# Kernel optimization log

Hardware: AMD Instinct MI355X
Metric: run time of the kernel (lower is better)

The kernel has to match this reference:

```python
import jax, jax.numpy as jnp
import numpy as np

N, E, F_IN, H, D = 50000, 800000, 256, 4, 128


def _gat_layer(x, W, al, ar, bias, src, dst):
    # x: [N, Fin]; W: [Fin, H*D]; al/ar: [H, D]; bias: [H*D]
    feat = (x @ W).reshape(N, H, D)                      # [N,H,D]
    el = jnp.einsum('nhd,hd->nh', feat, al)              # [N,H]
    er = jnp.einsum('nhd,hd->nh', feat, ar)              # [N,H]
    e = jax.nn.leaky_relu(el[src] + er[dst], negative_slope=0.2)  # [E,H]
    # edge softmax over incoming edges of each dst node (numerically stable)
    emax = jax.ops.segment_max(e, dst, num_segments=N)   # [N,H]
    ee = jnp.exp(e - emax[dst])                          # [E,H]
    denom = jax.ops.segment_sum(ee, dst, num_segments=N) # [N,H]
    a = ee / denom[dst]                                  # [E,H]
    # weighted scatter-aggregate of source features
    out = jax.ops.segment_sum(feat[src] * a[:, :, None], dst, num_segments=N)  # [N,H,D]
    return out + bias.reshape(H, D)


def setup_inputs() -> dict:
    key = jax.random.key(0)
    ks = jax.random.split(key, 16)
    f32 = jnp.float32
    nfeats = jax.random.normal(ks[0], (N, F_IN), dtype=f32)
    src = jax.random.randint(ks[1], (E,), 0, N, dtype=jnp.int32)
    dst = jax.random.randint(ks[2], (E,), 0, N, dtype=jnp.int32)
    def lin(k, fin):
        return jax.random.normal(k, (fin, H * D), dtype=f32) / np.sqrt(fin).astype(np.float32)
    def attn(k):
        return jax.random.normal(k, (H, D), dtype=f32) / np.sqrt(D).astype(np.float32)
    return {
        'nfeats': nfeats,
        'W1': lin(ks[3], F_IN), 'al1': attn(ks[4]), 'ar1': attn(ks[5]), 'b1': jnp.zeros((H * D,), f32),
        'W2': lin(ks[6], D),    'al2': attn(ks[7]), 'ar2': attn(ks[8]), 'b2': jnp.zeros((H * D,), f32),
        'W3': lin(ks[9], D),    'al3': attn(ks[10]), 'ar3': attn(ks[11]), 'b3': jnp.zeros((H * D,), f32),
        'Wc': jax.random.normal(ks[12], (D, 1), dtype=f32) / np.sqrt(D).astype(np.float32),
        'bc': jnp.zeros((1,), f32),
        'src': src, 'dst': dst,
    }


def reference(nfeats, W1, al1, ar1, b1, W2, al2, ar2, b2, W3, al3, ar3, b3, Wc, bc, src, dst):
    h = jnp.mean(jax.nn.relu(_gat_layer(nfeats, W1, al1, ar1, b1, src, dst)), axis=1)  # [N,D]
    h = jnp.mean(jax.nn.relu(_gat_layer(h, W2, al2, ar2, b2, src, dst)), axis=1)
    h = jnp.mean(jax.nn.relu(_gat_layer(h, W3, al3, ar3, b3, src, dst)), axis=1)
    hg = jnp.mean(h, axis=0, keepdims=True)  # readout: mean over nodes -> [1,D]
    return jax.nn.sigmoid(hg @ Wc + bc)      # [1,1]
```

## Files before the change

### kernel.cpp

```cpp
#include <hip/hip_runtime.h>
#include <hip/hip_bf16.h>

#define N_NODES 50000
#define E_EDGES 800000
#define HD 512
#define H_HEADS 4
#define D_DIM 128
#define N_PAD 53248

typedef __attribute__((ext_vector_type(8))) short bf16x8;
typedef __attribute__((ext_vector_type(4))) float f32x4;
typedef __attribute__((ext_vector_type(2))) float f32x2;

__device__ __forceinline__ unsigned short f2b(float f) {
  unsigned u = __float_as_uint(f);
  u += 0x7FFFu + ((u >> 16) & 1u);
  return (unsigned short)(u >> 16);
}
__device__ __forceinline__ float b2f(unsigned short s) {
  return __uint_as_float(((unsigned)s) << 16);
}
__device__ __forceinline__ float lrelu(float v) { return v > 0.f ? v : 0.2f * v; }
__device__ __forceinline__ float sel4(float a, float b, float c, float d, int h) {
  return h == 0 ? a : (h == 1 ? b : (h == 2 ? c : d));
}

#define GLOAD_LDS16(g, l)                                             \
  __builtin_amdgcn_global_load_lds(                                   \
      (const __attribute__((address_space(1))) void*)(g),             \
      (__attribute__((address_space(3))) void*)(l), 16, 0, 0)

__global__ void cast_f2b(const float* __restrict__ in, unsigned short* __restrict__ out, int n4) {
  int i = blockIdx.x * blockDim.x + threadIdx.x;
  if (i >= n4) return;
  float4 v = *(const float4*)(in + (size_t)i * 4);
  ushort4 o;
  o.x = f2b(v.x); o.y = f2b(v.y); o.z = f2b(v.z); o.w = f2b(v.w);
  *(ushort4*)(out + (size_t)i * 4) = o;
}

__global__ void transpose_cast(const float* __restrict__ W, unsigned short* __restrict__ WT, int K) {
  int idx = blockIdx.x * blockDim.x + threadIdx.x;
  if (idx >= K * HD) return;
  int k = idx >> 9, c = idx & (HD - 1);
  WT[(size_t)c * K + k] = f2b(W[idx]);
}

__global__ __launch_bounds__(256) void gemm_mfma(const unsigned short* __restrict__ X,
                                                 const unsigned short* __restrict__ WT,
                                                 unsigned short* __restrict__ feat, int K) {
  __shared__ unsigned short Atile[128 * 64];
  __shared__ unsigned short Btile[128 * 64];
  const int tid = threadIdx.x;
  const int w = tid >> 6, l = tid & 63;
  const int wr = w >> 1, wc = w & 1;
  const int row0 = blockIdx.x * 128;
  const int col0 = blockIdx.y * 128;
  const int fr = l & 15;
  const int fk = (l >> 4) * 8;
  f32x4 acc[4][4] = {};

  for (int k0 = 0; k0 < K; k0 += 64) {
#pragma unroll
    for (int j = 0; j < 4; ++j) {
      int idx = j * 256 + tid;
      int row = idx >> 3;
      int ksw = ((idx & 7) << 3) ^ ((row & 7) << 3);
      int arow = row0 + row;
      if (arow >= N_NODES) arow = N_NODES - 1;
      GLOAD_LDS16(X + (size_t)arow * K + k0 + ksw,
                  (char*)Atile + j * 4096 + w * 1024);
      GLOAD_LDS16(WT + (size_t)(col0 + row) * K + k0 + ksw,
                  (char*)Btile + j * 4096 + w * 1024);
    }
    __syncthreads();
#pragma unroll
    for (int kk = 0; kk < 64; kk += 32) {
      const int kel2 = (kk + fk) * 2;
      bf16x8 af[4], bf[4];
#pragma unroll
      for (int m = 0; m < 4; ++m) {
        int arow = wr * 64 + m * 16 + fr;
        af[m] = *(const bf16x8*)((const char*)Atile + arow * 128 + (kel2 ^ ((arow & 7) << 4)));
        int bcol = wc * 64 + m * 16 + fr;
        bf[m] = *(const bf16x8*)((const char*)Btile + bcol * 128 + (kel2 ^ ((bcol & 7) << 4)));
      }
#pragma unroll
      for (int m = 0; m < 4; ++m)
#pragma unroll
        for (int n = 0; n < 4; ++n)
          acc[m][n] = __builtin_amdgcn_mfma_f32_16x16x32_bf16(af[m], bf[n], acc[m][n], 0, 0, 0);
    }
    __syncthreads();
  }

  const int orow = row0 + wr * 64 + (l >> 4) * 4;
#pragma unroll
  for (int m = 0; m < 4; ++m) {
#pragma unroll
    for (int i = 0; i < 4; ++i) {
      int r = orow + m * 16 + i;
      if (r < N_NODES) {
#pragma unroll
        for (int n = 0; n < 4; ++n)
          feat[(size_t)r * HD + col0 + wc * 64 + n * 16 + fr] = f2b(acc[m][n][i]);
      }
    }
  }
}

__global__ __launch_bounds__(64) void eler_cast(const unsigned short* __restrict__ feat,
                                                const float* __restrict__ al,
                                                const float* __restrict__ ar,
                                                float* __restrict__ el, float* __restrict__ er,
                                                unsigned char* __restrict__ featq) {
  const int n = blockIdx.x, t = threadIdx.x;
  const int h = t >> 4, d0 = (t & 15) * 8;
  uint4 raw = *(const uint4*)(feat + (size_t)n * HD + t * 8);
  unsigned rw[4] = {raw.x, raw.y, raw.z, raw.w};
  float fv[8];
#pragma unroll
  for (int i = 0; i < 4; ++i) {
    fv[2 * i] = b2f((unsigned short)(rw[i] & 0xFFFFu));
    fv[2 * i + 1] = b2f((unsigned short)(rw[i] >> 16));
  }
  const float* alh = al + h * D_DIM + d0;
  const float* arh = ar + h * D_DIM + d0;
  float4 a0 = *(const float4*)alh, a1 = *(const float4*)(alh + 4);
  float4 r0 = *(const float4*)arh, r1 = *(const float4*)(arh + 4);
  float av[8] = {a0.x, a0.y, a0.z, a0.w, a1.x, a1.y, a1.z, a1.w};
  float rv[8] = {r0.x, r0.y, r0.z, r0.w, r1.x, r1.y, r1.z, r1.w};
  float sl = 0.f, sr = 0.f;
#pragma unroll
  for (int i = 0; i < 8; ++i) {
    sl = fmaf(fv[i], av[i], sl);
    sr = fmaf(fv[i], rv[i], sr);
  }
#pragma unroll
  for (int o = 1; o < 16; o <<= 1) {
    sl += __shfl_xor(sl, o);
    sr += __shfl_xor(sr, o);
  }
  if ((t & 15) == 0) {
    el[n * 4 + h] = sl;
    er[n * 4 + h] = sr;
  }
  int q0 = __builtin_amdgcn_cvt_pk_fp8_f32(fv[0], fv[1], 0, false);
  q0 = __builtin_amdgcn_cvt_pk_fp8_f32(fv[2], fv[3], q0, true);
  int q1 = __builtin_amdgcn_cvt_pk_fp8_f32(fv[4], fv[5], 0, false);
  q1 = __builtin_amdgcn_cvt_pk_fp8_f32(fv[6], fv[7], q1, true);
  uint2 qq;
  qq.x = (unsigned)q0;
  qq.y = (unsigned)q1;
  *(uint2*)(featq + (size_t)n * HD + t * 8) = qq;
}

__global__ void histo_kernel(const int* __restrict__ dst, unsigned* __restrict__ deg) {
  int e = blockIdx.x * blockDim.x + threadIdx.x;
  if (e >= E_EDGES) return;
  atomicAdd(&deg[dst[e]], 1u);
}

__global__ void scan_kernel(const unsigned* __restrict__ deg, unsigned* __restrict__ off,
                            unsigned* __restrict__ cursor) {
  __shared__ unsigned warp_sums[16];
  __shared__ unsigned carry_s;
  const int tid = threadIdx.x;
  const int wid = tid >> 6;
  if (tid == 0) carry_s = 0;
  __syncthreads();
  for (int base = 0; base < N_PAD; base += 4096) {
    int i = base + tid * 4;
    uint4 v = *(const uint4*)(deg + i);
    unsigned sm = v.x + v.y + v.z + v.w;
    unsigned x = sm;
#pragma unroll
    for (int o = 1; o < 64; o <<= 1) {
      unsigned y = __shfl_up(x, o);
      if ((tid & 63) >= o) x += y;
    }
    if ((tid & 63) == 63) warp_sums[wid] = x;
    __syncthreads();
    if (tid < 16) {
      unsigned s = warp_sums[tid];
#pragma unroll
      for (int o = 1; o < 16; o <<= 1) {
        unsigned y = __shfl_up(s, o);
        if (tid >= o) s += y;
      }
      warp_sums[tid] = s;
    }
    __syncthreads();
    unsigned carry = carry_s;
    unsigned wprev = (wid > 0) ? warp_sums[wid - 1] : 0u;
    unsigned ex = carry + wprev + (x - sm);
    uint4 o4;
    o4.x = ex;
    o4.y = ex + v.x;
    o4.z = o4.y + v.y;
    o4.w = o4.z + v.z;
    *(uint4*)(off + i) = o4;
    *(uint4*)(cursor + i) = o4;
    __syncthreads();
    if (tid == 0) carry_s = carry + warp_sums[15];
    __syncthreads();
  }
}

__global__ void scatter_kernel(const int* __restrict__ src, const int* __restrict__ dst,
                               unsigned* __restrict__ cursor, int* __restrict__ csr_src) {
  int e = blockIdx.x * blockDim.x + threadIdx.x;
  if (e >= E_EDGES) return;
  int d = dst[e];
  unsigned pos = atomicAdd(&cursor[d], 1u);
  csr_src[pos] = src[e];
}

__global__ __launch_bounds__(64) void agg_fused(const unsigned* __restrict__ off,
                                                const int* __restrict__ csr_src,
                                                const float* __restrict__ el,
                                                const float* __restrict__ er,
                                                const unsigned char* __restrict__ featq,
                                                const float* __restrict__ bias,
                                                unsigned short* __restrict__ hbuf) {
  __shared__ float4 ws4[64];
  const int n = blockIdx.x, t = threadIdx.x;
  const int h = t >> 4, d0 = (t & 15) * 8;
  const unsigned beg = off[n];
  const int deg = (int)(off[n + 1] - beg);
  const float NEG = -3.0e38f;
  float4 rr = *(const float4*)(er + (size_t)n * 4);
  float acc[8] = {};

  if (deg <= 64) {
    float4 v = {NEG, NEG, NEG, NEG};
    if (t < deg) {
      int s = csr_src[beg + t];
      float4 ll = *(const float4*)(el + (size_t)s * 4);
      v.x = lrelu(ll.x + rr.x);
      v.y = lrelu(ll.y + rr.y);
      v.z = lrelu(ll.z + rr.z);
      v.w = lrelu(ll.w + rr.w);
    }
    float m0 = v.x, m1 = v.y, m2 = v.z, m3 = v.w;
#pragma unroll
    for (int o = 32; o >= 1; o >>= 1) {
      m0 = fmaxf(m0, __shfl_xor(m0, o));
      m1 = fmaxf(m1, __shfl_xor(m1, o));
      m2 = fmaxf(m2, __shfl_xor(m2, o));
      m3 = fmaxf(m3, __shfl_xor(m3, o));
    }
    float4 ev = {0.f, 0.f, 0.f, 0.f};
    if (t < deg) {
      ev.x = __expf(v.x - m0);
      ev.y = __expf(v.y - m1);
      ev.z = __expf(v.z - m2);
      ev.w = __expf(v.w - m3);
    }
    float s0 = ev.x, s1 = ev.y, s2 = ev.z, s3 = ev.w;
#pragma unroll
    for (int o = 32; o >= 1; o >>= 1) {
      s0 += __shfl_xor(s0, o);
      s1 += __shfl_xor(s1, o);
      s2 += __shfl_xor(s2, o);
      s3 += __shfl_xor(s3, o);
    }
    if (t < deg) ws4[t] = ev;
    float invh = 1.0f / sel4(s0, s1, s2, s3, h);
    __syncthreads();
    int sj = (deg > 0) ? csr_src[beg] : 0;
    for (int j = 0; j < deg; ++j) {
      int sn = csr_src[beg + ((j + 1 < deg) ? j + 1 : j)];
      float4 wv = ws4[j];
      float w = sel4(wv.x, wv.y, wv.z, wv.w, h) * invh;
      uint2 q = *(const uint2*)(featq + (size_t)sj * HD + t * 8);
      f32x2 p0 = __builtin_amdgcn_cvt_pk_f32_fp8((int)q.x, false);
      f32x2 p1 = __builtin_amdgcn_cvt_pk_f32_fp8((int)q.x, true);
      f32x2 p2 = __builtin_amdgcn_cvt_pk_f32_fp8((int)q.y, false);
      f32x2 p3 = __builtin_amdgcn_cvt_pk_f32_fp8((int)q.y, true);
      acc[0] = fmaf(p0[0], w, acc[0]);
      acc[1] = fmaf(p0[1], w, acc[1]);
      acc[2] = fmaf(p1[0], w, acc[2]);
      acc[3] = fmaf(p1[1], w, acc[3]);
      acc[4] = fmaf(p2[0], w, acc[4]);
      acc[5] = fmaf(p2[1], w, acc[5]);
      acc[6] = fmaf(p3[0], w, acc[6]);
      acc[7] = fmaf(p3[1], w, acc[7]);
      sj = sn;
    }
  } else {
    float m[4] = {NEG, NEG, NEG, NEG};
    for (int j = t; j < deg; j += 64) {
      int s = csr_src[beg + j];
      float4 ll = *(const float4*)(el + (size_t)s * 4);
      m[0] = fmaxf(m[0], lrelu(ll.x + rr.x));
      m[1] = fmaxf(m[1], lrelu(ll.y + rr.y));
      m[2] = fmaxf(m[2], lrelu(ll.z + rr.z));
      m[3] = fmaxf(m[3], lrelu(ll.w + rr.w));
    }
#pragma unroll
    for (int o = 32; o >= 1; o >>= 1) {
      m[0] = fmaxf(m[0], __shfl_xor(m[0], o));
      m[1] = fmaxf(m[1], __shfl_xor(m[1], o));
      m[2] = fmaxf(m[2], __shfl_xor(m[2], o));
      m[3] = fmaxf(m[3], __shfl_xor(m[3], o));
    }
    float sm[4] = {0.f, 0.f, 0.f, 0.f};
    for (int j = t; j < deg; j += 64) {
      int s = csr_src[beg + j];
      float4 ll = *(const float4*)(el + (size_t)s * 4);
      sm[0] += __expf(lrelu(ll.x + rr.x) - m[0]);
      sm[1] += __expf(lrelu(ll.y + rr.y) - m[1]);
      sm[2] += __expf(lrelu(ll.z + rr.z) - m[2]);
      sm[3] += __expf(lrelu(ll.w + rr.w) - m[3]);
    }
#pragma unroll
    for (int o = 32; o >= 1; o >>= 1) {
      sm[0] += __shfl_xor(sm[0], o);
      sm[1] += __shfl_xor(sm[1], o);
      sm[2] += __shfl_xor(sm[2], o);
      sm[3] += __shfl_xor(sm[3], o);
    }
    float mh = sel4(m[0], m[1], m[2], m[3], h);
    float ih = 1.0f / sel4(sm[0], sm[1], sm[2], sm[3], h);
    float rrh = sel4(rr.x, rr.y, rr.z, rr.w, h);
    for (int j = 0; j < deg; ++j) {
      int sj = csr_src[beg + j];
      float llh = el[(size_t)sj * 4 + h];
      float w = __expf(lrelu(llh + rrh) - mh) * ih;
      uint2 q = *(const uint2*)(featq + (size_t)sj * HD + t * 8);
      f32x2 p0 = __builtin_amdgcn_cvt_pk_f32_fp8((int)q.x, false);
      f32x2 p1 = __builtin_amdgcn_cvt_pk_f32_fp8((int)q.x, true);
      f32x2 p2 = __builtin_amdgcn_cvt_pk_f32_fp8((int)q.y, false);
      f32x2 p3 = __builtin_amdgcn_cvt_pk_f32_fp8((int)q.y, true);
      acc[0] = fmaf(p0[0], w, acc[0]);
      acc[1] = fmaf(p0[1], w, acc[1]);
      acc[2] = fmaf(p1[0], w, acc[2]);
      acc[3] = fmaf(p1[1], w, acc[3]);
      acc[4] = fmaf(p2[0], w, acc[4]);
      acc[5] = fmaf(p2[1], w, acc[5]);
      acc[6] = fmaf(p3[0], w, acc[6]);
      acc[7] = fmaf(p3[1], w, acc[7]);
    }
  }

  const float* bp = bias + h * D_DIM + d0;
  float4 b0 = *(const float4*)bp, b1 = *(const float4*)(bp + 4);
  float bv[8] = {b0.x, b0.y, b0.z, b0.w, b1.x, b1.y, b1.z, b1.w};
  float r[8];
#pragma unroll
  for (int i = 0; i < 8; ++i) r[i] = fmaxf(acc[i] + bv[i], 0.f);
#pragma unroll
  for (int i = 0; i < 8; ++i) {
    r[i] += __shfl_xor(r[i], 16);
    r[i] += __shfl_xor(r[i], 32);
  }
  if (h == 0) {
    uint4 o;
    o.x = (unsigned)f2b(r[0] * 0.25f) | ((unsigned)f2b(r[1] * 0.25f) << 16);
    o.y = (unsigned)f2b(r[2] * 0.25f) | ((unsigned)f2b(r[3] * 0.25f) << 16);
    o.z = (unsigned)f2b(r[4] * 0.25f) | ((unsigned)f2b(r[5] * 0.25f) << 16);
    o.w = (unsigned)f2b(r[6] * 0.25f) | ((unsigned)f2b(r[7] * 0.25f) << 16);
    *(uint4*)(hbuf + (size_t)n * D_DIM + d0) = o;
  }
}

__global__ void colsum(const unsigned short* __restrict__ hbuf, float* __restrict__ hg) {
  int d = threadIdx.x;
  float s = 0.0f;
  for (int n = blockIdx.x; n < N_NODES; n += gridDim.x)
    s += b2f(hbuf[(size_t)n * D_DIM + d]);
  atomicAdd(&hg[d], s);
}

__global__ void final_k(const float* __restrict__ hg, const float* __restrict__ Wc,
                        const float* __restrict__ bc, float* __restrict__ out) {
  int l = threadIdx.x;
  float v = hg[l] * Wc[l] + hg[l + 64] * Wc[l + 64];
#pragma unroll
  for (int off = 32; off >= 1; off >>= 1) v += __shfl_xor(v, off);
  if (l == 0) {
    float x = v * (1.0f / N_NODES) + bc[0];
    out[0] = 1.0f / (1.0f + expf(-x));
  }
}

extern "C" void kernel_launch(void* const* d_in, const int* in_sizes, int n_in,
                              void* d_out, int out_size, void* d_ws, size_t ws_size,
                              hipStream_t stream) {
  const float* nfeats = (const float*)d_in[0];
  const float* W1 = (const float*)d_in[1];
  const float* al1 = (const float*)d_in[2];
  const float* ar1 = (const float*)d_in[3];
  const float* b1 = (const float*)d_in[4];
  const float* W2 = (const float*)d_in[5];
  const float* al2 = (const float*)d_in[6];
  const float* ar2 = (const float*)d_in[7];
  const float* b2 = (const float*)d_in[8];
  const float* W3 = (const float*)d_in[9];
  const float* al3 = (const float*)d_in[10];
  const float* ar3 = (const float*)d_in[11];
  const float* b3 = (const float*)d_in[12];
  const float* Wc = (const float*)d_in[13];
  const float* bc = (const float*)d_in[14];
  const int* src = (const int*)d_in[15];
  const int* dst = (const int*)d_in[16];
  float* out = (float*)d_out;

  char* p = (char*)d_ws;
  auto carve = [&](size_t bytes) {
    char* r = p;
    p += (bytes + 255) & ~(size_t)255;
    return r;
  };
  float* el = (float*)carve((size_t)N_NODES * 4 * 4);
  float* er = (float*)carve((size_t)N_NODES * 4 * 4);
  float* hg = (float*)carve(512);
  unsigned* deg = (unsigned*)carve((size_t)N_PAD * 4);
  unsigned* offv = (unsigned*)carve((size_t)(N_PAD + 4) * 4);
  unsigned* cursor = (unsigned*)carve((size_t)N_PAD * 4);
  int* csr_src = (int*)carve((size_t)E_EDGES * 4);
  unsigned short* featb = (unsigned short*)carve((size_t)N_NODES * HD * 2);
  unsigned char* featq = (unsigned char*)carve((size_t)N_NODES * HD);
  unsigned short* hbufb = (unsigned short*)carve((size_t)N_NODES * D_DIM * 2);
  unsigned short* xb = (unsigned short*)carve((size_t)(N_NODES + 128) * 256 * 2);
  unsigned short* WT1 = (unsigned short*)carve((size_t)HD * 256 * 2);
  unsigned short* WT2 = (unsigned short*)carve((size_t)HD * 128 * 2);
  unsigned short* WT3 = (unsigned short*)carve((size_t)HD * 128 * 2);

  hipMemsetAsync(deg, 0, (size_t)N_PAD * sizeof(unsigned), stream);
  histo_kernel<<<(E_EDGES + 255) / 256, 256, 0, stream>>>(dst, deg);
  scan_kernel<<<1, 1024, 0, stream>>>(deg, offv, cursor);
  scatter_kernel<<<(E_EDGES + 255) / 256, 256, 0, stream>>>(src, dst, cursor, csr_src);

  cast_f2b<<<(N_NODES * 256 / 4 + 255) / 256, 256, 0, stream>>>(nfeats, xb, N_NODES * 256 / 4);
  transpose_cast<<<(256 * HD + 255) / 256, 256, 0, stream>>>(W1, WT1, 256);
  transpose_cast<<<(128 * HD + 255) / 256, 256, 0, stream>>>(W2, WT2, 128);
  transpose_cast<<<(128 * HD + 255) / 256, 256, 0, stream>>>(W3, WT3, 128);

  auto run_layer = [&](const unsigned short* X, int K, const unsigned short* WT,
                       const float* alv, const float* arv, const float* bv) {
    dim3 g((N_NODES + 127) / 128, HD / 128);
    gemm_mfma<<<g, 256, 0, stream>>>(X, WT, featb, K);
    eler_cast<<<N_NODES, 64, 0, stream>>>(featb, alv, arv, el, er, featq);
    agg_fused<<<N_NODES, 64, 0, stream>>>(offv, csr_src, el, er, featq, bv, hbufb);
  };

  run_layer(xb, 256, WT1, al1, ar1, b1);
  run_layer(hbufb, 128, WT2, al2, ar2, b2);
  run_layer(hbufb, 128, WT3, al3, ar3, b3);

  hipMemsetAsync(hg, 0, 512, stream);
  colsum<<<1024, 128, 0, stream>>>(hbufb, hg);
  final_k<<<1, 64, 0, stream>>>(hg, Wc, bc, out);
}
```

Baseline: 491.9 us.

## Fold attention vectors into weights, quantize GEMM output to fp8 directly, unroll aggregation

Precomputes W·al and W·ar per layer so el/er come from a small GEMV over the input features, and deletes the eler_cast kernel along with the bf16 feature buffer. The GEMM epilogue now writes fp8 features directly, cutting a full write and re-read of the bf16 feature matrix. The low-degree aggregation loop is unrolled by 4 with independent gathers and packed f32x2 FMAs to raise memory-level parallelism. The GEMM now stores single bytes, which may coalesce poorly, and el/er are computed from bf16 inputs instead of bf16-rounded features, which slightly changes the numerics.

```diff
diff --git a/kernel.cpp b/kernel.cpp
--- a/kernel.cpp
+++ b/kernel.cpp
@@ -23,6 +23,9 @@
 __device__ __forceinline__ float lrelu(float v) { return v > 0.f ? v : 0.2f * v; }
 __device__ __forceinline__ float sel4(float a, float b, float c, float d, int h) {
   return h == 0 ? a : (h == 1 ? b : (h == 2 ? c : d));
+}
+__device__ __forceinline__ float sel4v(float4 v, int h) {
+  return sel4(v.x, v.y, v.z, v.w, h);
 }
 
 #define GLOAD_LDS16(g, l)                                             \
@@ -46,9 +49,71 @@
   WT[(size_t)c * K + k] = f2b(W[idx]);
 }
 
+__global__ void compute_wal(const float* __restrict__ W, const float* __restrict__ al,
+                            const float* __restrict__ ar, float* __restrict__ wal, int K) {
+  int idx = blockIdx.x * blockDim.x + threadIdx.x;
+  if (idx >= K * 8) return;
+  int k = idx >> 3, j = idx & 7, h = j >> 1;
+  const float* a = ((j & 1) ? ar : al) + h * D_DIM;
+  const float* w = W + (size_t)k * HD + h * D_DIM;
+  float s = 0.f;
+  for (int d = 0; d < D_DIM; d += 4) {
+    float4 wv = *(const float4*)(w + d);
+    float4 av = *(const float4*)(a + d);
+    s = fmaf(wv.x, av.x, s);
+    s = fmaf(wv.y, av.y, s);
+    s = fmaf(wv.z, av.z, s);
+    s = fmaf(wv.w, av.w, s);
+  }
+  wal[idx] = s;
+}
+
+__global__ __launch_bounds__(256) void gemv_eler(const unsigned short* __restrict__ X,
+                                                 const float* __restrict__ wal,
+                                                 float* __restrict__ el, float* __restrict__ er,
+                                                 int K) {
+  const int t = threadIdx.x;
+  const int u = (t & 63) >> 3, v = t & 7;
+  const int wave = t >> 6;
+  const int n0 = blockIdx.x * 32 + wave * 8 + u;
+  int n = (n0 < N_NODES) ? n0 : N_NODES - 1;
+  const int kc = K >> 3;
+  const unsigned short* xp = X + (size_t)n * K + v * kc;
+  float acc[8] = {};
+  for (int k = 0; k < kc; k += 8) {
+    bf16x8 xv = *(const bf16x8*)(xp + k);
+    int kg = v * kc + k;
+#pragma unroll
+    for (int i = 0; i < 8; ++i) {
+      float xf = b2f((unsigned short)xv[i]);
+      float4 w0 = *(const float4*)(wal + (size_t)(kg + i) * 8);
+      float4 w1 = *(const float4*)(wal + (size_t)(kg + i) * 8 + 4);
+      acc[0] = fmaf(xf, w0.x, acc[0]);
+      acc[1] = fmaf(xf, w0.y, acc[1]);
+      acc[2] = fmaf(xf, w0.z, acc[2]);
+      acc[3] = fmaf(xf, w0.w, acc[3]);
+      acc[4] = fmaf(xf, w1.x, acc[4]);
+      acc[5] = fmaf(xf, w1.y, acc[5]);
+      acc[6] = fmaf(xf, w1.z, acc[6]);
+      acc[7] = fmaf(xf, w1.w, acc[7]);
+    }
+  }
+#pragma unroll
+  for (int o = 1; o < 8; o <<= 1) {
+#pragma unroll
+    for (int j = 0; j < 8; ++j) acc[j] += __shfl_xor(acc[j], o);
+  }
+  if (v == 0 && n0 < N_NODES) {
+    float4 elv = {acc[0], acc[2], acc[4], acc[6]};
+    float4 erv = {acc[1], acc[3], acc[5], acc[7]};
+    *(float4*)(el + (size_t)n0 * 4) = elv;
+    *(float4*)(er + (size_t)n0 * 4) = erv;
+  }
+}
+
 __global__ __launch_bounds__(256) void gemm_mfma(const unsigned short* __restrict__ X,
                                                  const unsigned short* __restrict__ WT,
-                                                 unsigned short* __restrict__ feat, int K) {
+                                                 unsigned char* __restrict__ featq, int K) {
   __shared__ unsigned short Atile[128 * 64];
   __shared__ unsigned short Btile[128 * 64];
   const int tid = threadIdx.x;
@@ -94,65 +159,22 @@
     __syncthreads();
   }
 
-  const int orow = row0 + wr * 64 + (l >> 4) * 4;
+  const int g = l >> 4;
+  const int col_base = col0 + wc * 64;
 #pragma unroll
   for (int m = 0; m < 4; ++m) {
 #pragma unroll
     for (int i = 0; i < 4; ++i) {
-      int r = orow + m * 16 + i;
+      int r = row0 + wr * 64 + m * 16 + g * 4 + i;
       if (r < N_NODES) {
 #pragma unroll
-        for (int n = 0; n < 4; ++n)
-          feat[(size_t)r * HD + col0 + wc * 64 + n * 16 + fr] = f2b(acc[m][n][i]);
+        for (int n = 0; n < 4; ++n) {
+          int b = __builtin_amdgcn_cvt_pk_fp8_f32(acc[m][n][i], acc[m][n][i], 0, false);
+          featq[(size_t)r * HD + col_base + n * 16 + fr] = (unsigned char)(b & 0xFF);
+        }
       }
     }
   }
-}
-
-__global__ __launch_bounds__(64) void eler_cast(const unsigned short* __restrict__ feat,
-                                                const float* __restrict__ al,
-                                                const float* __restrict__ ar,
-                                                float* __restrict__ el, float* __restrict__ er,
-                                                unsigned char* __restrict__ featq) {
-  const int n = blockIdx.x, t = threadIdx.x;
-  const int h = t >> 4, d0 = (t & 15) * 8;
-  uint4 raw = *(const uint4*)(feat + (size_t)n * HD + t * 8);
-  unsigned rw[4] = {raw.x, raw.y, raw.z, raw.w};
-  float fv[8];
-#pragma unroll
-  for (int i = 0; i < 4; ++i) {
-    fv[2 * i] = b2f((unsigned short)(rw[i] & 0xFFFFu));
-    fv[2 * i + 1] = b2f((unsigned short)(rw[i] >> 16));
-  }
-  const float* alh = al + h * D_DIM + d0;
-  const float* arh = ar + h * D_DIM + d0;
-  float4 a0 = *(const float4*)alh, a1 = *(const float4*)(alh + 4);
-  float4 r0 = *(const float4*)arh, r1 = *(const float4*)(arh + 4);
-  float av[8] = {a0.x, a0.y, a0.z, a0.w, a1.x, a1.y, a1.z, a1.w};
-  float rv[8] = {r0.x, r0.y, r0.z, r0.w, r1.x, r1.y, r1.z, r1.w};
-  float sl = 0.f, sr = 0.f;
-#pragma unroll
-  for (int i = 0; i < 8; ++i) {
-    sl = fmaf(fv[i], av[i], sl);
-    sr = fmaf(fv[i], rv[i], sr);
-  }
-#pragma unroll
-  for (int o = 1; o < 16; o <<= 1) {
-    sl += __shfl_xor(sl, o);
-    sr += __shfl_xor(sr, o);
-  }
-  if ((t & 15) == 0) {
-    el[n * 4 + h] = sl;
-    er[n * 4 + h] = sr;
-  }
-  int q0 = __builtin_amdgcn_cvt_pk_fp8_f32(fv[0], fv[1], 0, false);
-  q0 = __builtin_amdgcn_cvt_pk_fp8_f32(fv[2], fv[3], q0, true);
-  int q1 = __builtin_amdgcn_cvt_pk_fp8_f32(fv[4], fv[5], 0, false);
-  q1 = __builtin_amdgcn_cvt_pk_fp8_f32(fv[6], fv[7], q1, true);
-  uint2 qq;
-  qq.x = (unsigned)q0;
-  qq.y = (unsigned)q1;
-  *(uint2*)(featq + (size_t)n * HD + t * 8) = qq;
 }
 
 __global__ void histo_kernel(const int* __restrict__ dst, unsigned* __restrict__ deg) {
@@ -230,7 +252,7 @@
   const int deg = (int)(off[n + 1] - beg);
   const float NEG = -3.0e38f;
   float4 rr = *(const float4*)(er + (size_t)n * 4);
-  float acc[8] = {};
+  f32x2 acc2[4] = {};
 
   if (deg <= 64) {
     float4 v = {NEG, NEG, NEG, NEG};
@@ -265,28 +287,48 @@
       s2 += __shfl_xor(s2, o);
       s3 += __shfl_xor(s3, o);
     }
-    if (t < deg) ws4[t] = ev;
+    ws4[t] = ev;
     float invh = 1.0f / sel4(s0, s1, s2, s3, h);
     __syncthreads();
-    int sj = (deg > 0) ? csr_src[beg] : 0;
-    for (int j = 0; j < deg; ++j) {
-      int sn = csr_src[beg + ((j + 1 < deg) ? j + 1 : j)];
-      float4 wv = ws4[j];
-      float w = sel4(wv.x, wv.y, wv.z, wv.w, h) * invh;
-      uint2 q = *(const uint2*)(featq + (size_t)sj * HD + t * 8);
-      f32x2 p0 = __builtin_amdgcn_cvt_pk_f32_fp8((int)q.x, false);
-      f32x2 p1 = __builtin_amdgcn_cvt_pk_f32_fp8((int)q.x, true);
-      f32x2 p2 = __builtin_amdgcn_cvt_pk_f32_fp8((int)q.y, false);
-      f32x2 p3 = __builtin_amdgcn_cvt_pk_f32_fp8((int)q.y, true);
-      acc[0] = fmaf(p0[0], w, acc[0]);
-      acc[1] = fmaf(p0[1], w, acc[1]);
-      acc[2] = fmaf(p1[0], w, acc[2]);
-      acc[3] = fmaf(p1[1], w, acc[3]);
-      acc[4] = fmaf(p2[0], w, acc[4]);
-      acc[5] = fmaf(p2[1], w, acc[5]);
-      acc[6] = fmaf(p3[0], w, acc[6]);
-      acc[7] = fmaf(p3[1], w, acc[7]);
-      sj = sn;
+    const unsigned char* fq = featq + t * 8;
+    for (int j0 = 0; j0 < deg; j0 += 4) {
+      int i1 = (j0 + 1 < deg) ? j0 + 1 : j0;
+      int i2 = (j0 + 2 < deg) ? j0 + 2 : j0;
+      int i3 = (j0 + 3 < deg) ? j0 + 3 : j0;
+      int sa = csr_src[beg + j0], sb = csr_src[beg + i1];
+      int sc = csr_src[beg + i2], sd = csr_src[beg + i3];
+      uint2 qa = *(const uint2*)(fq + (size_t)sa * HD);
+      uint2 qb = *(const uint2*)(fq + (size_t)sb * HD);
+      uint2 qc = *(const uint2*)(fq + (size_t)sc * HD);
+      uint2 qd = *(const uint2*)(fq + (size_t)sd * HD);
+      float wa = sel4v(ws4[j0], h) * invh;
+      float wb = sel4v(ws4[i1], h) * invh;
+      float wc2 = sel4v(ws4[i2], h) * invh;
+      float wd = sel4v(ws4[i3], h) * invh;
+      if (j0 + 1 >= deg) wb = 0.f;
+      if (j0 + 2 >= deg) wc2 = 0.f;
+      if (j0 + 3 >= deg) wd = 0.f;
+      f32x2 w2;
+      w2 = (f32x2){wa, wa};
+      acc2[0] += __builtin_amdgcn_cvt_pk_f32_fp8((int)qa.x, false) * w2;
+      acc2[1] += __builtin_amdgcn_cvt_pk_f32_fp8((int)qa.x, true) * w2;
+      acc2[2] += __builtin_amdgcn_cvt_pk_f32_fp8((int)qa.y, false) * w2;
+      acc2[3] += __builtin_amdgcn_cvt_pk_f32_fp8((int)qa.y, true) * w2;
+      w2 = (f32x2){wb, wb};
+      acc2[0] += __builtin_amdgcn_cvt_pk_f32_fp8((int)qb.x, false) * w2;
+      acc2[1] += __builtin_amdgcn_cvt_pk_f32_fp8((int)qb.x, true) * w2;
+      acc2[2] += __builtin_amdgcn_cvt_pk_f32_fp8((int)qb.y, false) * w2;
+      acc2[3] += __builtin_amdgcn_cvt_pk_f32_fp8((int)qb.y, true) * w2;
+      w2 = (f32x2){wc2, wc2};
+      acc2[0] += __builtin_amdgcn_cvt_pk_f32_fp8((int)qc.x, false) * w2;
+      acc2[1] += __builtin_amdgcn_cvt_pk_f32_fp8((int)qc.x, true) * w2;
+      acc2[2] += __builtin_amdgcn_cvt_pk_f32_fp8((int)qc.y, false) * w2;
+      acc2[3] += __builtin_amdgcn_cvt_pk_f32_fp8((int)qc.y, true) * w2;
+      w2 = (f32x2){wd, wd};
+      acc2[0] += __builtin_amdgcn_cvt_pk_f32_fp8((int)qd.x, false) * w2;
+      acc2[1] += __builtin_amdgcn_cvt_pk_f32_fp8((int)qd.x, true) * w2;
+      acc2[2] += __builtin_amdgcn_cvt_pk_f32_fp8((int)qd.y, false) * w2;
+      acc2[3] += __builtin_amdgcn_cvt_pk_f32_fp8((int)qd.y, true) * w2;
     }
   } else {
     float m[4] = {NEG, NEG, NEG, NEG};
@@ -329,18 +371,11 @@
       float llh = el[(size_t)sj * 4 + h];
       float w = __expf(lrelu(llh + rrh) - mh) * ih;
       uint2 q = *(const uint2*)(featq + (size_t)sj * HD + t * 8);
-      f32x2 p0 = __builtin_amdgcn_cvt_pk_f32_fp8((int)q.x, false);
-      f32x2 p1 = __builtin_amdgcn_cvt_pk_f32_fp8((int)q.x, true);
-      f32x2 p2 = __builtin_amdgcn_cvt_pk_f32_fp8((int)q.y, false);
-      f32x2 p3 = __builtin_amdgcn_cvt_pk_f32_fp8((int)q.y, true);
-      acc[0] = fmaf(p0[0], w, acc[0]);
-      acc[1] = fmaf(p0[1], w, acc[1]);
-      acc[2] = fmaf(p1[0], w, acc[2]);
-      acc[3] = fmaf(p1[1], w, acc[3]);
-      acc[4] = fmaf(p2[0], w, acc[4]);
-      acc[5] = fmaf(p2[1], w, acc[5]);
-      acc[6] = fmaf(p3[0], w, acc[6]);
-      acc[7] = fmaf(p3[1], w, acc[7]);
+      f32x2 w2 = {w, w};
+      acc2[0] += __builtin_amdgcn_cvt_pk_f32_fp8((int)q.x, false) * w2;
+      acc2[1] += __builtin_amdgcn_cvt_pk_f32_fp8((int)q.x, true) * w2;
+      acc2[2] += __builtin_amdgcn_cvt_pk_f32_fp8((int)q.y, false) * w2;
+      acc2[3] += __builtin_amdgcn_cvt_pk_f32_fp8((int)q.y, true) * w2;
     }
   }
 
@@ -349,7 +384,7 @@
   float bv[8] = {b0.x, b0.y, b0.z, b0.w, b1.x, b1.y, b1.z, b1.w};
   float r[8];
 #pragma unroll
-  for (int i = 0; i < 8; ++i) r[i] = fmaxf(acc[i] + bv[i], 0.f);
+  for (int i = 0; i < 8; ++i) r[i] = fmaxf(acc2[i >> 1][i & 1] + bv[i], 0.f);
 #pragma unroll
   for (int i = 0; i < 8; ++i) {
     r[i] += __shfl_xor(r[i], 16);
@@ -420,13 +455,15 @@
   unsigned* offv = (unsigned*)carve((size_t)(N_PAD + 4) * 4);
   unsigned* cursor = (unsigned*)carve((size_t)N_PAD * 4);
   int* csr_src = (int*)carve((size_t)E_EDGES * 4);
-  unsigned short* featb = (unsigned short*)carve((size_t)N_NODES * HD * 2);
   unsigned char* featq = (unsigned char*)carve((size_t)N_NODES * HD);
   unsigned short* hbufb = (unsigned short*)carve((size_t)N_NODES * D_DIM * 2);
   unsigned short* xb = (unsigned short*)carve((size_t)(N_NODES + 128) * 256 * 2);
   unsigned short* WT1 = (unsigned short*)carve((size_t)HD * 256 * 2);
   unsigned short* WT2 = (unsigned short*)carve((size_t)HD * 128 * 2);
   unsigned short* WT3 = (unsigned short*)carve((size_t)HD * 128 * 2);
+  float* wal1 = (float*)carve((size_t)256 * 8 * 4);
+  float* wal2 = (float*)carve((size_t)128 * 8 * 4);
+  float* wal3 = (float*)carve((size_t)128 * 8 * 4);
 
   hipMemsetAsync(deg, 0, (size_t)N_PAD * sizeof(unsigned), stream);
   histo_kernel<<<(E_EDGES + 255) / 256, 256, 0, stream>>>(dst, deg);
@@ -437,18 +474,21 @@
   transpose_cast<<<(256 * HD + 255) / 256, 256, 0, stream>>>(W1, WT1, 256);
   transpose_cast<<<(128 * HD + 255) / 256, 256, 0, stream>>>(W2, WT2, 128);
   transpose_cast<<<(128 * HD + 255) / 256, 256, 0, stream>>>(W3, WT3, 128);
+  compute_wal<<<(256 * 8 + 255) / 256, 256, 0, stream>>>(W1, al1, ar1, wal1, 256);
+  compute_wal<<<(128 * 8 + 255) / 256, 256, 0, stream>>>(W2, al2, ar2, wal2, 128);
+  compute_wal<<<(128 * 8 + 255) / 256, 256, 0, stream>>>(W3, al3, ar3, wal3, 128);
 
   auto run_layer = [&](const unsigned short* X, int K, const unsigned short* WT,
-                       const float* alv, const float* arv, const float* bv) {
+                       const float* wal, const float* bv) {
     dim3 g((N_NODES + 127) / 128, HD / 128);
-    gemm_mfma<<<g, 256, 0, stream>>>(X, WT, featb, K);
-    eler_cast<<<N_NODES, 64, 0, stream>>>(featb, alv, arv, el, er, featq);
+    gemm_mfma<<<g, 256, 0, stream>>>(X, WT, featq, K);
+    gemv_eler<<<(N_NODES + 31) / 32, 256, 0, stream>>>(X, wal, el, er, K);
     agg_fused<<<N_NODES, 64, 0, stream>>>(offv, csr_src, el, er, featq, bv, hbufb);
   };
 
-  run_layer(xb, 256, WT1, al1, ar1, b1);
-  run_layer(hbufb, 128, WT2, al2, ar2, b2);
-  run_layer(hbufb, 128, WT3, al3, ar3, b3);
+  run_layer(xb, 256, WT1, wal1, b1);
+  run_layer(hbufb, 128, WT2, wal2, b2);
+  run_layer(hbufb, 128, WT3, wal3, b3);
 
   hipMemsetAsync(hg, 0, 512, stream);
   colsum<<<1024, 128, 0, stream>>>(hbufb, hg);
```

Measured after the change: 558.2 us. +13.5%, slower.
